# Optimization experiments

Hardware: AMD Instinct MI355X
Metric: run time of the kernel (lower is better)

## Reference

```python
import jax, jax.numpy as jnp
import numpy as np

EMBED_DIM = 1024
NUM_HEADS = 16
HEAD_DIM = EMBED_DIM // NUM_HEADS


def setup_inputs() -> dict:
    key = jax.random.key(0)
    ks = jax.random.split(key, 9)
    B, T, C = 2, 2048, EMBED_DIM
    s = 1.0 / np.sqrt(C)
    inp = {
        "x": jax.random.normal(ks[0], (B, T, C), dtype=jnp.float32),
        "Wq": jax.random.uniform(ks[1], (C, C), jnp.float32, -s, s),
        "bq": jax.random.uniform(ks[2], (C,), jnp.float32, -s, s),
        "Wk": jax.random.uniform(ks[3], (C, C), jnp.float32, -s, s),
        "bk": jax.random.uniform(ks[4], (C,), jnp.float32, -s, s),
        "Wv": jax.random.uniform(ks[5], (C, C), jnp.float32, -s, s),
        "bv": jax.random.uniform(ks[6], (C,), jnp.float32, -s, s),
        "Wo": jax.random.uniform(ks[7], (C, C), jnp.float32, -s, s),
        "bo": jax.random.uniform(ks[8], (C,), jnp.float32, -s, s),
    }
    return inp


def reference(x, Wq, bq, Wk, bk, Wv, bv, Wo, bo):
    B, T, C = x.shape
    H, D = NUM_HEADS, HEAD_DIM

    def heads(W, b):
        # [B,T,C] -> [B,H,T,D]
        return (x @ W + b).reshape(B, T, H, D).transpose(0, 2, 1, 3)

    q = heads(Wq, bq)
    k = heads(Wk, bk)
    v = heads(Wv, bv)

    scores = jnp.einsum('bhtd,bhsd->bhts', q, k) / np.sqrt(D).astype(np.float32)
    causal = jnp.tril(jnp.ones((T, T), dtype=bool))  # [T,T]
    scores = jnp.where(causal[None, None], scores, -jnp.inf)
    weights = jax.nn.softmax(scores, axis=-1)
    out = jnp.einsum('bhts,bhsd->bhtd', weights, v)  # [B,H,T,D]
    out = out.transpose(0, 2, 1, 3).reshape(B, T, C)
    return out @ Wo + bo
```

## Files before the change

### kernel.cpp

```cpp
#include <hip/hip_runtime.h>
#include <stdint.h>

#define T_LEN 2048
#define C_DIM 1024
#define NHEAD 16
#define HDIM  64
#define MTOT  4096

typedef __bf16 bf16;
typedef __bf16 bf16x4 __attribute__((ext_vector_type(4)));
typedef __bf16 bf16x8 __attribute__((ext_vector_type(8)));
typedef float  f32x4  __attribute__((ext_vector_type(4)));

__device__ __forceinline__ bf16 f2bf(float f) {
    union { float f; unsigned u; } x; x.f = f;
    unsigned r = x.u + 0x7fffu + ((x.u >> 16) & 1u);
    unsigned short h = (unsigned short)(r >> 16);
    return __builtin_bit_cast(bf16, h);
}

__device__ __forceinline__ void g2l16(const void* g, const void* l) {
    __builtin_amdgcn_global_load_lds(
        (const __attribute__((address_space(1))) unsigned int*)(uintptr_t)g,
        (__attribute__((address_space(3))) unsigned int*)(uint32_t)(uintptr_t)l,
        16, 0, 0);
}


__global__ void cast_x_kernel(const float* __restrict__ x, bf16* __restrict__ xb) {
    int f = blockIdx.x * 256 + threadIdx.x;
    const float4* p = (const float4*)x + (size_t)f * 2;
    float4 a = p[0], b = p[1];
    bf16x8 o;
    o[0] = f2bf(a.x); o[1] = f2bf(a.y); o[2] = f2bf(a.z); o[3] = f2bf(a.w);
    o[4] = f2bf(b.x); o[5] = f2bf(b.y); o[6] = f2bf(b.z); o[7] = f2bf(b.w);
    ((bf16x8*)xb)[f] = o;
}

__global__ void cast_w_kernel(const float* __restrict__ W0, const float* __restrict__ W1,
                              const float* __restrict__ W2, const float* __restrict__ W3,
                              bf16* __restrict__ wt) {
    __shared__ float tile[64][68];
    const int tid = threadIdx.x;
    const int w = blockIdx.z;
    const float* W = (w == 0) ? W0 : (w == 1) ? W1 : (w == 2) ? W2 : W3;
    const int kb = blockIdx.x * 64, nb = blockIdx.y * 64;
#pragma unroll
    for (int pass = 0; pass < 4; ++pass) {
        int row = pass * 16 + (tid >> 4);
        int col = (tid & 15) * 4;
        float4 v = *(const float4*)(W + (size_t)(kb + row) * 1024 + nb + col);
        *(float4*)(&tile[row][col]) = v;
    }
    __syncthreads();
#pragma unroll
    for (int pass = 0; pass < 2; ++pass) {
        int s = pass * 256 + tid;
        int nn = s >> 3, c = s & 7;
        bf16x8 o;
#pragma unroll
        for (int j = 0; j < 8; ++j) o[j] = f2bf(tile[c * 8 + j][nn]);
        *(bf16x8*)(wt + (size_t)w * 1048576 + (size_t)(nb + nn) * 1024 + kb + c * 8) = o;
    }
}

__global__ void transpose_v_kernel(const bf16* __restrict__ V, bf16* __restrict__ Vtp) {
    __shared__ bf16 tile[128][72];
    const int tid = threadIdx.x;
    const int t0 = blockIdx.x * 128, bh = blockIdx.y;
    const size_t hb = (size_t)bh * 131072;
#pragma unroll
    for (int pass = 0; pass < 4; ++pass) {
        int s = pass * 256 + tid;
        int row = s >> 3, c = s & 7;
        bf16x8 v = *(const bf16x8*)(V + hb + (size_t)(t0 + row) * 64 + c * 8);
        *(bf16x8*)(&tile[row][c * 8]) = v;
    }
    __syncthreads();
#pragma unroll
    for (int pass = 0; pass < 4; ++pass) {
        int s = pass * 256 + tid;
        int d = s >> 4, ch = s & 15;
        bf16x8 o;
#pragma unroll
        for (int j = 0; j < 8; ++j) {
            int orig = 32 * (ch >> 2) + 16 * (j >> 2) + 4 * (ch & 3) + (j & 3);
            o[j] = tile[orig][d];
        }
        *(bf16x8*)(Vtp + hb + (size_t)d * 2048 + t0 + ch * 8) = o;
    }
}

__global__ __launch_bounds__(256, 2)
void gemm_bt_kernel(const bf16* __restrict__ A, const bf16* __restrict__ WtAll,
                    const float* __restrict__ b0, const float* __restrict__ b1,
                    const float* __restrict__ b2, bf16* __restrict__ outQKV) {
    __shared__ char lds[32768];
    bf16* As = (bf16*)lds;
    bf16* Bs = (bf16*)(lds + 16384);

    const int tid = threadIdx.x;
    const int lane = tid & 63, wid = tid >> 6;
    const int r = lane & 15, q4 = lane >> 4;
    const int mbase = blockIdx.y * 128;
    const int nbase = blockIdx.x * 128;
    const int z = blockIdx.z;
    const bf16* Bt = WtAll + (size_t)z * 1048576;
    const float* bias = (z == 0) ? b0 : (z == 1) ? b1 : b2;
    const float osc = (z == 0) ? 0.18033688011112042f : 1.0f;

    const int wm = (wid >> 1) * 64;
    const int wn = (wid & 1) * 64;

    float4 bvv[4];
#pragma unroll
    for (int j = 0; j < 4; ++j) bvv[j] = *(const float4*)(bias + nbase + wn + j * 16 + q4 * 4);

    f32x4 acc[4][4];
#pragma unroll
    for (int i = 0; i < 4; ++i)
#pragma unroll
        for (int j = 0; j < 4; ++j) acc[i][j] = f32x4{0.f, 0.f, 0.f, 0.f};

    for (int kt = 0; kt < 16; ++kt) {
        int kb = kt * 64;
#pragma unroll
        for (int p = 0; p < 4; ++p) {
            int s = p * 256 + tid;
            int row = s >> 3, blk = s & 7;
            int sb = blk ^ (row & 7);
            g2l16(A  + (size_t)(mbase + row) * 1024 + kb + sb * 8, (char*)As + s * 16);
            g2l16(Bt + (size_t)(nbase + row) * 1024 + kb + sb * 8, (char*)Bs + s * 16);
        }
        __syncthreads();
#pragma unroll
        for (int ks = 0; ks < 2; ++ks) {
            int blk = ks * 4 + q4;
            bf16x8 a[4], b[4];
#pragma unroll
            for (int i = 0; i < 4; ++i) {
                int rowa = wm + i * 16 + r;
                a[i] = *(const bf16x8*)((const char*)As + rowa * 128 + ((blk ^ (rowa & 7)) * 16));
                int rowb = wn + i * 16 + r;
                b[i] = *(const bf16x8*)((const char*)Bs + rowb * 128 + ((blk ^ (rowb & 7)) * 16));
            }
#pragma unroll
            for (int i = 0; i < 4; ++i)
#pragma unroll
                for (int j = 0; j < 4; ++j)
                    acc[i][j] = __builtin_amdgcn_mfma_f32_16x16x32_bf16(b[j], a[i], acc[i][j], 0, 0, 0);
        }
        __syncthreads();
    }

#pragma unroll
    for (int i = 0; i < 4; ++i) {
        int m = mbase + wm + i * 16 + r;
        int bi = m >> 11, t = m & 2047;
#pragma unroll
        for (int j = 0; j < 4; ++j) {
            int n0 = nbase + wn + j * 16 + q4 * 4;
            bf16x4 w;
            w[0] = f2bf((acc[i][j][0] + bvv[j].x) * osc);
            w[1] = f2bf((acc[i][j][1] + bvv[j].y) * osc);
            w[2] = f2bf((acc[i][j][2] + bvv[j].z) * osc);
            w[3] = f2bf((acc[i][j][3] + bvv[j].w) * osc);
            int h = n0 >> 6, d = n0 & 63;
            *(bf16x4*)(outQKV + (size_t)z * 4194304 + ((size_t)(bi * 16 + h) * 2048 + t) * 64 + d) = w;
        }
    }
}

__global__ __launch_bounds__(256, 2)
void gemm_o_kernel(const bf16* __restrict__ A, const bf16* __restrict__ Bt,
                   const float* __restrict__ bias, float* __restrict__ out) {
    __shared__ char lds[24576];
    bf16* As = (bf16*)lds;
    bf16* Bs = (bf16*)(lds + 16384);

    const int tid = threadIdx.x;
    const int lane = tid & 63, wid = tid >> 6;
    const int r = lane & 15, q4 = lane >> 4;
    const int nb = blockIdx.x * 64;
    const int mb = blockIdx.y * 128;
    const int wm = (wid >> 1) * 64;
    const int wn = (wid & 1) * 32;

    float4 bvv[2];
#pragma unroll
    for (int j = 0; j < 2; ++j) bvv[j] = *(const float4*)(bias + nb + wn + j * 16 + q4 * 4);

    f32x4 acc[4][2];
#pragma unroll
    for (int i = 0; i < 4; ++i)
#pragma unroll
        for (int j = 0; j < 2; ++j) acc[i][j] = f32x4{0.f, 0.f, 0.f, 0.f};

    for (int kt = 0; kt < 16; ++kt) {
        int kb = kt * 64;
#pragma unroll
        for (int p = 0; p < 4; ++p) {
            int s = p * 256 + tid;
            int row = s >> 3, blk = s & 7;
            g2l16(A + (size_t)(mb + row) * 1024 + kb + ((blk ^ (row & 7)) * 8), (char*)As + s * 16);
        }
#pragma unroll
        for (int p = 0; p < 2; ++p) {
            int s = p * 256 + tid;
            int row = s >> 3, blk = s & 7;
            g2l16(Bt + (size_t)(nb + row) * 1024 + kb + ((blk ^ (row & 7)) * 8), (char*)Bs + s * 16);
        }
        __syncthreads();
#pragma unroll
        for (int ks = 0; ks < 2; ++ks) {
            int blk = ks * 4 + q4;
            bf16x8 a[4], b[2];
#pragma unroll
            for (int i = 0; i < 4; ++i) {
                int rowa = wm + i * 16 + r;
                a[i] = *(const bf16x8*)((const char*)As + rowa * 128 + ((blk ^ (rowa & 7)) * 16));
            }
#pragma unroll
            for (int j = 0; j < 2; ++j) {
                int rowb = wn + j * 16 + r;
                b[j] = *(const bf16x8*)((const char*)Bs + rowb * 128 + ((blk ^ (rowb & 7)) * 16));
            }
#pragma unroll
            for (int i = 0; i < 4; ++i)
#pragma unroll
                for (int j = 0; j < 2; ++j)
                    acc[i][j] = __builtin_amdgcn_mfma_f32_16x16x32_bf16(b[j], a[i], acc[i][j], 0, 0, 0);
        }
        __syncthreads();
    }

#pragma unroll
    for (int i = 0; i < 4; ++i) {
        int m = mb + wm + i * 16 + r;
#pragma unroll
        for (int j = 0; j < 2; ++j) {
            int n0 = nb + wn + j * 16 + q4 * 4;
            float4 w;
            w.x = acc[i][j][0] + bvv[j].x;
            w.y = acc[i][j][1] + bvv[j].y;
            w.z = acc[i][j][2] + bvv[j].z;
            w.w = acc[i][j][3] + bvv[j].w;
            *(float4*)(out + (size_t)m * 1024 + n0) = w;
        }
    }
}

__global__ __launch_bounds__(512, 2)
void attn_kernel(const bf16* __restrict__ Q, const bf16* __restrict__ K,
                 const bf16* __restrict__ Vtp, bf16* __restrict__ Aout) {
    __shared__ char lds[65536];

    const int tid = threadIdx.x, lane = tid & 63, wid = tid >> 6;
    const int r = lane & 15, q4 = lane >> 4;
    const int p = blockIdx.x >> 5;
    const int bh = blockIdx.x & 31;
    const int b = bh >> 4, h = bh & 15;
    const size_t hb = (size_t)bh * 131072;

    const int qi[2] = { p, 15 - p };
    const int ittot = 16 - p;

    bf16x8 qf[2][2];
#pragma unroll
    for (int i = 0; i < 2; ++i)
#pragma unroll
        for (int ks = 0; ks < 2; ++ks) {
            int row = qi[i] * 128 + wid * 16 + r;
            qf[i][ks] = *(const bf16x8*)(Q + hb + (size_t)row * 64 + ks * 32 + q4 * 8);
        }

    bf16x8 ones;
#pragma unroll
    for (int j = 0; j < 8; ++j) ones[j] = (bf16)1.0f;

    f32x4 o[2][4];
    f32x4 osum[2];
#pragma unroll
    for (int i = 0; i < 2; ++i) {
        osum[i] = f32x4{0.f, 0.f, 0.f, 0.f};
#pragma unroll
        for (int jd = 0; jd < 4; ++jd) o[i][jd] = f32x4{0.f, 0.f, 0.f, 0.f};
    }

    auto stage = [&](int buf, int kb) {
        char* Kb = lds + buf * 16384;
        char* Vb = lds + 32768 + buf * 16384;
#pragma unroll
        for (int pp = 0; pp < 2; ++pp) {
            int s = pp * 512 + tid;
            int row = s >> 3, blk = s & 7;
            g2l16(K + hb + (size_t)(kb + row) * 64 + ((blk ^ (row & 7)) * 8), Kb + s * 16);
        }
#pragma unroll
        for (int pp = 0; pp < 2; ++pp) {
            int s = pp * 512 + tid;
            int row = s >> 4, ch = s & 15;
            g2l16(Vtp + hb + (size_t)row * 2048 + kb + ((ch ^ (row & 15)) * 8), Vb + s * 16);
        }
    };

    stage(0, 0);

    for (int it = 0; it < ittot; ++it) {
        __syncthreads();
        const int cb = it & 1;
        if (it + 1 < ittot) stage((it + 1) & 1, (it + 1) * 128);
        const int kb = it * 128;
        const char* Kb = lds + cb * 16384;
        const char* Vb = lds + 32768 + cb * 16384;
        const bool aAct = (it <= qi[0]);

        f32x4 sc[2][8];
#pragma unroll
        for (int st = 0; st < 8; ++st) {
            int rowk = st * 16 + r;
            bf16x8 ak0 = *(const bf16x8*)(Kb + rowk * 128 + ((q4 ^ (rowk & 7)) * 16));
            bf16x8 ak1 = *(const bf16x8*)(Kb + rowk * 128 + (((4 + q4) ^ (rowk & 7)) * 16));
            sc[1][st] = __builtin_amdgcn_mfma_f32_16x16x32_bf16(ak0, qf[1][0], f32x4{0.f, 0.f, 0.f, 0.f}, 0, 0, 0);
            sc[1][st] = __builtin_amdgcn_mfma_f32_16x16x32_bf16(ak1, qf[1][1], sc[1][st], 0, 0, 0);
            if (aAct) {
                sc[0][st] = __builtin_amdgcn_mfma_f32_16x16x32_bf16(ak0, qf[0][0], f32x4{0.f, 0.f, 0.f, 0.f}, 0, 0, 0);
                sc[0][st] = __builtin_amdgcn_mfma_f32_16x16x32_bf16(ak1, qf[0][1], sc[0][st], 0, 0, 0);
            }
        }

#pragma unroll
        for (int i = 0; i < 2; ++i) {
            if (i == 0 && !aAct) continue;
            const bool dia = (it == qi[i]);
            int qrow = qi[i] * 128 + wid * 16 + r;
            bf16x8 pb[4];
#pragma unroll
            for (int c = 0; c < 4; ++c) {
                bf16x8 t;
                if (dia) {
#pragma unroll
                    for (int j = 0; j < 8; ++j) {
                        int st = 2 * c + (j >> 2), reg = j & 3;
                        int key = kb + st * 16 + q4 * 4 + reg;
                        float sv = (key > qrow) ? -1e30f : sc[i][st][reg];
                        t[j] = (bf16)__builtin_amdgcn_exp2f(sv);
                    }
                } else {
#pragma unroll
                    for (int j = 0; j < 8; ++j) {
                        int st = 2 * c + (j >> 2), reg = j & 3;
                        t[j] = (bf16)__builtin_amdgcn_exp2f(sc[i][st][reg]);
                    }
                }
                pb[c] = t;
            }
#pragma unroll
            for (int c = 0; c < 4; ++c) {
                int sidx = c * 4 + q4;
                osum[i] = __builtin_amdgcn_mfma_f32_16x16x32_bf16(ones, pb[c], osum[i], 0, 0, 0);
#pragma unroll
                for (int dsub = 0; dsub < 4; ++dsub) {
                    int rowd = dsub * 16 + r;
                    bf16x8 av = *(const bf16x8*)(Vb + rowd * 256 + ((sidx ^ (rowd & 15)) * 16));
                    o[i][dsub] = __builtin_amdgcn_mfma_f32_16x16x32_bf16(av, pb[c], o[i][dsub], 0, 0, 0);
                }
            }
        }
    }

#pragma unroll
    for (int i = 0; i < 2; ++i) {
        float inv = 1.f / osum[i][0];
        int q = qi[i] * 128 + wid * 16 + r;
#pragma unroll
        for (int dsub = 0; dsub < 4; ++dsub) {
            bf16x4 w;
#pragma unroll
            for (int reg = 0; reg < 4; ++reg) w[reg] = f2bf(o[i][dsub][reg] * inv);
            *(bf16x4*)(Aout + ((size_t)(b * 2048 + q)) * 1024 + h * 64 + dsub * 16 + q4 * 4) = w;
        }
    }
}


extern "C" void kernel_launch(void* const* d_in, const int* in_sizes, int n_in,
                              void* d_out, int out_size, void* d_ws, size_t ws_size,
                              hipStream_t stream) {
    const float* x  = (const float*)d_in[0];
    const float* Wq = (const float*)d_in[1];
    const float* bq = (const float*)d_in[2];
    const float* Wk = (const float*)d_in[3];
    const float* bk = (const float*)d_in[4];
    const float* Wv = (const float*)d_in[5];
    const float* bv = (const float*)d_in[6];
    const float* Wo = (const float*)d_in[7];
    const float* bo = (const float*)d_in[8];
    float* out = (float*)d_out;

    char* ws = (char*)d_ws;
    bf16* xb   = (bf16*)(ws);
    bf16* wt   = (bf16*)(ws + 8388608);
    bf16* qkv  = (bf16*)(ws + 16777216);
    bf16* vtp  = (bf16*)(ws + 41943040);
    bf16* attn = (bf16*)(ws + 50331648);

    hipLaunchKernelGGL(cast_x_kernel, dim3(2048), dim3(256), 0, stream, x, xb);
    hipLaunchKernelGGL(cast_w_kernel, dim3(16, 16, 4), dim3(256), 0, stream, Wq, Wk, Wv, Wo, wt);
    hipLaunchKernelGGL(gemm_bt_kernel, dim3(8, 32, 3), dim3(256), 0, stream,
                       xb, wt, bq, bk, bv, qkv);
    hipLaunchKernelGGL(transpose_v_kernel, dim3(16, 32), dim3(256), 0, stream,
                       qkv + (size_t)2 * 4194304, vtp);
    hipLaunchKernelGGL(attn_kernel, dim3(256), dim3(512), 0, stream,
                       qkv, qkv + 4194304, vtp, attn);
    hipLaunchKernelGGL(gemm_o_kernel, dim3(16, 32), dim3(256), 0, stream,
                       attn, wt + (size_t)3 * 1048576, bo, out);
}
```

Before: 176.8 us.

## Merge cast kernels and widen QKV GEMM tile to 128x192 over fused weights

The x-cast and weight-cast kernels become one launch that dispatches on block index. The QKV projection now treats Wq/Wk/Wv as one contiguous 3072-wide transposed weight and uses 128x192 tiles (6 MFMA columns per wave), giving 512 blocks instead of 768. The bias and Q scale are picked per output column in the epilogue. This cuts a launch and reuses each A tile across more output columns, at the cost of more accumulator registers and 40KB of LDS, which may lower occupancy.

```diff
diff --git a/kernel.cpp b/kernel.cpp
--- a/kernel.cpp
+++ b/kernel.cpp
@@ -26,25 +26,29 @@
         16, 0, 0);
 }
 
-
-__global__ void cast_x_kernel(const float* __restrict__ x, bf16* __restrict__ xb) {
-    int f = blockIdx.x * 256 + threadIdx.x;
-    const float4* p = (const float4*)x + (size_t)f * 2;
-    float4 a = p[0], b = p[1];
-    bf16x8 o;
-    o[0] = f2bf(a.x); o[1] = f2bf(a.y); o[2] = f2bf(a.z); o[3] = f2bf(a.w);
-    o[4] = f2bf(b.x); o[5] = f2bf(b.y); o[6] = f2bf(b.z); o[7] = f2bf(b.w);
-    ((bf16x8*)xb)[f] = o;
-}
-
-__global__ void cast_w_kernel(const float* __restrict__ W0, const float* __restrict__ W1,
-                              const float* __restrict__ W2, const float* __restrict__ W3,
-                              bf16* __restrict__ wt) {
+__global__ void cast_xw_kernel(const float* __restrict__ x, bf16* __restrict__ xb,
+                               const float* __restrict__ W0, const float* __restrict__ W1,
+                               const float* __restrict__ W2, const float* __restrict__ W3,
+                               bf16* __restrict__ wt) {
     __shared__ float tile[64][68];
     const int tid = threadIdx.x;
-    const int w = blockIdx.z;
+    const int bid = blockIdx.x;
+    if (bid < 2048) {
+        int f = bid * 256 + tid;
+        const float4* p = (const float4*)x + (size_t)f * 2;
+        float4 a = p[0], b = p[1];
+        bf16x8 o;
+        o[0] = f2bf(a.x); o[1] = f2bf(a.y); o[2] = f2bf(a.z); o[3] = f2bf(a.w);
+        o[4] = f2bf(b.x); o[5] = f2bf(b.y); o[6] = f2bf(b.z); o[7] = f2bf(b.w);
+        ((bf16x8*)xb)[f] = o;
+        return;
+    }
+    const int i = bid - 2048;
+    const int w = i >> 8;
+    const int nt = (i >> 4) & 15;
+    const int kt = i & 15;
     const float* W = (w == 0) ? W0 : (w == 1) ? W1 : (w == 2) ? W2 : W3;
-    const int kb = blockIdx.x * 64, nb = blockIdx.y * 64;
+    const int kb = kt * 64, nb = nt * 64;
 #pragma unroll
     for (int pass = 0; pass < 4; ++pass) {
         int row = pass * 16 + (tid >> 4);
@@ -92,10 +96,10 @@
 }
 
 __global__ __launch_bounds__(256, 2)
-void gemm_bt_kernel(const bf16* __restrict__ A, const bf16* __restrict__ WtAll,
-                    const float* __restrict__ b0, const float* __restrict__ b1,
-                    const float* __restrict__ b2, bf16* __restrict__ outQKV) {
-    __shared__ char lds[32768];
+void gemm_qkv_kernel(const bf16* __restrict__ A, const bf16* __restrict__ Wt,
+                     const float* __restrict__ b0, const float* __restrict__ b1,
+                     const float* __restrict__ b2, bf16* __restrict__ outQKV) {
+    __shared__ char lds[40960];
     bf16* As = (bf16*)lds;
     bf16* Bs = (bf16*)(lds + 16384);
 
@@ -103,24 +107,15 @@
     const int lane = tid & 63, wid = tid >> 6;
     const int r = lane & 15, q4 = lane >> 4;
     const int mbase = blockIdx.y * 128;
-    const int nbase = blockIdx.x * 128;
-    const int z = blockIdx.z;
-    const bf16* Bt = WtAll + (size_t)z * 1048576;
-    const float* bias = (z == 0) ? b0 : (z == 1) ? b1 : b2;
-    const float osc = (z == 0) ? 0.18033688011112042f : 1.0f;
-
+    const int nbase = blockIdx.x * 192;
     const int wm = (wid >> 1) * 64;
-    const int wn = (wid & 1) * 64;
-
-    float4 bvv[4];
-#pragma unroll
-    for (int j = 0; j < 4; ++j) bvv[j] = *(const float4*)(bias + nbase + wn + j * 16 + q4 * 4);
-
-    f32x4 acc[4][4];
+    const int wn = (wid & 1) * 96;
+
+    f32x4 acc[4][6];
 #pragma unroll
     for (int i = 0; i < 4; ++i)
 #pragma unroll
-        for (int j = 0; j < 4; ++j) acc[i][j] = f32x4{0.f, 0.f, 0.f, 0.f};
+        for (int j = 0; j < 6; ++j) acc[i][j] = f32x4{0.f, 0.f, 0.f, 0.f};
 
     for (int kt = 0; kt < 16; ++kt) {
         int kb = kt * 64;
@@ -128,44 +123,57 @@
         for (int p = 0; p < 4; ++p) {
             int s = p * 256 + tid;
             int row = s >> 3, blk = s & 7;
-            int sb = blk ^ (row & 7);
-            g2l16(A  + (size_t)(mbase + row) * 1024 + kb + sb * 8, (char*)As + s * 16);
-            g2l16(Bt + (size_t)(nbase + row) * 1024 + kb + sb * 8, (char*)Bs + s * 16);
+            g2l16(A + (size_t)(mbase + row) * 1024 + kb + ((blk ^ (row & 7)) * 8), (char*)As + s * 16);
+        }
+#pragma unroll
+        for (int p = 0; p < 6; ++p) {
+            int s = p * 256 + tid;
+            int row = s >> 3, blk = s & 7;
+            g2l16(Wt + (size_t)(nbase + row) * 1024 + kb + ((blk ^ (row & 7)) * 8), (char*)Bs + s * 16);
         }
         __syncthreads();
 #pragma unroll
         for (int ks = 0; ks < 2; ++ks) {
             int blk = ks * 4 + q4;
-            bf16x8 a[4], b[4];
+            bf16x8 a[4], b[6];
 #pragma unroll
             for (int i = 0; i < 4; ++i) {
                 int rowa = wm + i * 16 + r;
                 a[i] = *(const bf16x8*)((const char*)As + rowa * 128 + ((blk ^ (rowa & 7)) * 16));
-                int rowb = wn + i * 16 + r;
-                b[i] = *(const bf16x8*)((const char*)Bs + rowb * 128 + ((blk ^ (rowb & 7)) * 16));
+            }
+#pragma unroll
+            for (int j = 0; j < 6; ++j) {
+                int rowb = wn + j * 16 + r;
+                b[j] = *(const bf16x8*)((const char*)Bs + rowb * 128 + ((blk ^ (rowb & 7)) * 16));
             }
 #pragma unroll
             for (int i = 0; i < 4; ++i)
 #pragma unroll
-                for (int j = 0; j < 4; ++j)
+                for (int j = 0; j < 6; ++j)
                     acc[i][j] = __builtin_amdgcn_mfma_f32_16x16x32_bf16(b[j], a[i], acc[i][j], 0, 0, 0);
         }
         __syncthreads();
     }
 
+    const float QS = 0.18033688011112042f;
 #pragma unroll
     for (int i = 0; i < 4; ++i) {
         int m = mbase + wm + i * 16 + r;
         int bi = m >> 11, t = m & 2047;
 #pragma unroll
-        for (int j = 0; j < 4; ++j) {
+        for (int j = 0; j < 6; ++j) {
             int n0 = nbase + wn + j * 16 + q4 * 4;
+            int z = n0 >> 10;
+            int nz = n0 & 1023;
+            const float* bias = (z == 0) ? b0 : (z == 1) ? b1 : b2;
+            float4 bb = *(const float4*)(bias + nz);
+            float osc = (z == 0) ? QS : 1.0f;
             bf16x4 w;
-            w[0] = f2bf((acc[i][j][0] + bvv[j].x) * osc);
-            w[1] = f2bf((acc[i][j][1] + bvv[j].y) * osc);
-            w[2] = f2bf((acc[i][j][2] + bvv[j].z) * osc);
-            w[3] = f2bf((acc[i][j][3] + bvv[j].w) * osc);
-            int h = n0 >> 6, d = n0 & 63;
+            w[0] = f2bf((acc[i][j][0] + bb.x) * osc);
+            w[1] = f2bf((acc[i][j][1] + bb.y) * osc);
+            w[2] = f2bf((acc[i][j][2] + bb.z) * osc);
+            w[3] = f2bf((acc[i][j][3] + bb.w) * osc);
+            int h = nz >> 6, d = nz & 63;
             *(bf16x4*)(outQKV + (size_t)z * 4194304 + ((size_t)(bi * 16 + h) * 2048 + t) * 64 + d) = w;
         }
     }
@@ -405,9 +413,9 @@
     bf16* vtp  = (bf16*)(ws + 41943040);
     bf16* attn = (bf16*)(ws + 50331648);
 
-    hipLaunchKernelGGL(cast_x_kernel, dim3(2048), dim3(256), 0, stream, x, xb);
-    hipLaunchKernelGGL(cast_w_kernel, dim3(16, 16, 4), dim3(256), 0, stream, Wq, Wk, Wv, Wo, wt);
-    hipLaunchKernelGGL(gemm_bt_kernel, dim3(8, 32, 3), dim3(256), 0, stream,
+    hipLaunchKernelGGL(cast_xw_kernel, dim3(3072), dim3(256), 0, stream,
+                       x, xb, Wq, Wk, Wv, Wo, wt);
+    hipLaunchKernelGGL(gemm_qkv_kernel, dim3(16, 32), dim3(256), 0, stream,
                        xb, wt, bq, bk, bv, qkv);
     hipLaunchKernelGGL(transpose_v_kernel, dim3(16, 32), dim3(256), 0, stream,
                        qkv + (size_t)2 * 4194304, vtp);
```

After: 171.1 us. 3.2% less time.
